# Performance work log

Hardware: AMD Instinct MI355X
Metric: run time of the kernel (lower is better)

The kernel has to match this reference:

```python
import jax, jax.numpy as jnp
import numpy as np

HEAD_DIM = 64  # scale = head_dim ** -0.5


def setup_inputs() -> dict:
    key = jax.random.key(0)
    ks = jax.random.split(key, 5)
    B, S, E = 8, 8192, 1024
    L, D = 64, 256          # n_latent_vec, latent_dim
    H = HEAD_DIM
    return {
        "input_tensor": jax.random.normal(ks[0], (B, S, E), dtype=jnp.float32),
        "latents": jax.random.normal(ks[1], (L, D), dtype=jnp.float32),
        "Wq": jax.random.normal(ks[2], (H, D), dtype=jnp.float32) * (1.0 / np.sqrt(D)),
        "Wk": jax.random.normal(ks[3], (H, E), dtype=jnp.float32) * (1.0 / np.sqrt(E)),
        "Wv": jax.random.normal(ks[4], (H, E), dtype=jnp.float32) * (1.0 / np.sqrt(E)),
    }


def reference(input_tensor, latents, Wq, Wk, Wv):
    # non-cached path, seq_len == max_seq_len so no truncation
    # queries: broadcast shared latents over batch -> [B, L, H]
    q = jnp.einsum('ld,hd->lh', latents, Wq)                 # [L, H]
    k = jnp.einsum('bse,he->bsh', input_tensor, Wk)           # [B, S, H]
    v = jnp.einsum('bse,he->bsh', input_tensor, Wv)           # [B, S, H]
    scale = HEAD_DIM ** -0.5
    scores = jnp.einsum('lh,bsh->bls', q, k) * scale          # [B, L, S]
    weights = jax.nn.softmax(scores, axis=-1)                 # dropout is identity (p=0 / eval)
    out = jnp.einsum('bls,bsh->blh', weights, v)              # [B, L, H]
    return out
```

## Files before the change

### kernel.cpp

```cpp
#include <hip/hip_runtime.h>
#include <stdint.h>


typedef __attribute__((__ext_vector_type__(4))) float f32x4;
typedef __attribute__((__ext_vector_type__(8))) short bf16x8;

__device__ __forceinline__ unsigned short f2bf(float f) {
    union { float f; uint32_t u; } v; v.f = f;
    uint32_t u = v.u;
    return (unsigned short)((u + 0x7fffu + ((u >> 16) & 1u)) >> 16);
}

__global__ __launch_bounds__(256) void prep_kernel(
    const float* __restrict__ latents, const float* __restrict__ Wq,
    const float* __restrict__ Wk, const float* __restrict__ Wv,
    unsigned short* __restrict__ wkv, unsigned short* __restrict__ qbf)
{
    const int blk = blockIdx.x, tid = threadIdx.x;
    if (blk < 128) {
        const float* src = (blk < 64) ? (Wk + (size_t)blk * 1024)
                                      : (Wv + (size_t)(blk - 64) * 1024);
        for (int i = tid; i < 1024; i += 256)
            wkv[(size_t)blk * 1024 + i] = f2bf(src[i]);
    } else {
        const int l = (blk - 128) * 4 + (tid >> 6);
        const int h = tid & 63;
        float a = 0.f;
        for (int d = 0; d < 256; ++d)
            a += latents[l * 256 + d] * Wq[h * 256 + d];
        qbf[l * 64 + h] = f2bf(a * 0.125f);
    }
}

__global__ __launch_bounds__(256) void fused_kernel(
    const float* __restrict__ x, const unsigned short* __restrict__ wkv,
    const unsigned short* __restrict__ qbf,
    float* __restrict__ Opart, float* __restrict__ mpart, float* __restrict__ spart)
{
    __shared__ unsigned short smem[33792];
    unsigned short* Ab = smem;
    unsigned short* Bb = smem + 10240;
    unsigned short* Cs = smem;
    unsigned short* qs = smem + 20480;
    unsigned short* Ps = smem + 25088;
    __shared__ float red[4][64];
    __shared__ float Mrow[64];

    const int tid = threadIdx.x;
    const int wave = tid >> 6, lane = tid & 63;
    const int g = lane >> 4, c = lane & 15;
    const int wr = wave >> 1, wc = wave & 1;
    const size_t r0 = (size_t)blockIdx.x * 128;

    {
        const int rowQ = tid >> 3, colQ = (tid & 7) * 8;
        #pragma unroll
        for (int i = 0; i < 2; ++i) {
            const int row = rowQ + 32 * i;
            *(uint4*)&qs[row * 72 + colQ] = *(const uint4*)(qbf + row * 64 + colQ);
        }
    }

    const int rowA = tid >> 3, colA = (tid & 7) * 4;
    const int rowB = tid >> 2, colB = (tid & 3) * 8;

    f32x4 acc[4][4];
    #pragma unroll
    for (int i = 0; i < 4; ++i)
        #pragma unroll
        for (int j = 0; j < 4; ++j)
            acc[i][j] = f32x4{0.f, 0.f, 0.f, 0.f};

    f32x4 areg[4];
    uint4  breg[2];

    #pragma unroll
    for (int i = 0; i < 4; ++i)
        areg[i] = *(const f32x4*)(x + (r0 + rowA + 32 * i) * 1024 + colA);
    #pragma unroll
    for (int j = 0; j < 2; ++j)
        breg[j] = *(const uint4*)(wkv + (size_t)(rowB + 64 * j) * 1024 + colB);
    #pragma unroll
    for (int i = 0; i < 4; ++i) {
        unsigned long long pk =
            (unsigned long long)f2bf(areg[i][0])        |
            ((unsigned long long)f2bf(areg[i][1]) << 16) |
            ((unsigned long long)f2bf(areg[i][2]) << 32) |
            ((unsigned long long)f2bf(areg[i][3]) << 48);
        *(unsigned long long*)&Ab[(rowA + 32 * i) * 40 + colA] = pk;
    }
    #pragma unroll
    for (int j = 0; j < 2; ++j)
        *(uint4*)&Bb[(rowB + 64 * j) * 40 + colB] = breg[j];
    __syncthreads();

    for (int t = 0; t < 32; ++t) {
        const int buf = t & 1;
        if (t < 31) {
            const int e0 = (t + 1) * 32;
            #pragma unroll
            for (int i = 0; i < 4; ++i)
                areg[i] = *(const f32x4*)(x + (r0 + rowA + 32 * i) * 1024 + e0 + colA);
            #pragma unroll
            for (int j = 0; j < 2; ++j)
                breg[j] = *(const uint4*)(wkv + (size_t)(rowB + 64 * j) * 1024 + e0 + colB);
        }
        bf16x8 af[4], bfr[4];
        #pragma unroll
        for (int ml = 0; ml < 4; ++ml)
            af[ml] = *(const bf16x8*)&Ab[(buf * 128 + 64 * wr + 16 * ml + c) * 40 + 8 * g];
        #pragma unroll
        for (int nc = 0; nc < 4; ++nc)
            bfr[nc] = *(const bf16x8*)&Bb[(buf * 128 + 64 * wc + 16 * nc + c) * 40 + 8 * g];
        #pragma unroll
        for (int ml = 0; ml < 4; ++ml)
            #pragma unroll
            for (int nc = 0; nc < 4; ++nc)
                acc[ml][nc] = __builtin_amdgcn_mfma_f32_16x16x32_bf16(
                    af[ml], bfr[nc], acc[ml][nc], 0, 0, 0);
        if (t < 31) {
            const int nb = buf ^ 1;
            #pragma unroll
            for (int i = 0; i < 4; ++i) {
                unsigned long long pk =
                    (unsigned long long)f2bf(areg[i][0])        |
                    ((unsigned long long)f2bf(areg[i][1]) << 16) |
                    ((unsigned long long)f2bf(areg[i][2]) << 32) |
                    ((unsigned long long)f2bf(areg[i][3]) << 48);
                *(unsigned long long*)&Ab[(nb * 128 + rowA + 32 * i) * 40 + colA] = pk;
            }
            #pragma unroll
            for (int j = 0; j < 2; ++j)
                *(uint4*)&Bb[(nb * 128 + rowB + 64 * j) * 40 + colB] = breg[j];
        }
        __syncthreads();
    }

    #pragma unroll
    for (int ml = 0; ml < 4; ++ml)
        #pragma unroll
        for (int nc = 0; nc < 4; ++nc)
            #pragma unroll
            for (int r = 0; r < 4; ++r)
                Cs[(64 * wr + 16 * ml + 4 * g + r) * 136 + 64 * wc + 16 * nc + c] =
                    f2bf(acc[ml][nc][r]);
    __syncthreads();

    f32x4 sc[4][2];
    #pragma unroll
    for (int ml = 0; ml < 4; ++ml)
        #pragma unroll
        for (int ns = 0; ns < 2; ++ns)
            sc[ml][ns] = f32x4{0.f, 0.f, 0.f, 0.f};
    #pragma unroll
    for (int k0 = 0; k0 < 2; ++k0) {
        bf16x8 aq[4];
        #pragma unroll
        for (int ml = 0; ml < 4; ++ml)
            aq[ml] = *(const bf16x8*)&qs[(16 * ml + c) * 72 + 32 * k0 + 8 * g];
        #pragma unroll
        for (int ns = 0; ns < 2; ++ns) {
            bf16x8 bk = *(const bf16x8*)&Cs[(32 * wave + 16 * ns + c) * 136 + 32 * k0 + 8 * g];
            #pragma unroll
            for (int ml = 0; ml < 4; ++ml)
                sc[ml][ns] = __builtin_amdgcn_mfma_f32_16x16x32_bf16(
                    aq[ml], bk, sc[ml][ns], 0, 0, 0);
        }
    }

    float mloc[4][4];
    #pragma unroll
    for (int ml = 0; ml < 4; ++ml)
        #pragma unroll
        for (int r = 0; r < 4; ++r)
            mloc[ml][r] = fmaxf(sc[ml][0][r], sc[ml][1][r]);
    #pragma unroll
    for (int off = 1; off <= 8; off <<= 1)
        #pragma unroll
        for (int ml = 0; ml < 4; ++ml)
            #pragma unroll
            for (int r = 0; r < 4; ++r)
                mloc[ml][r] = fmaxf(mloc[ml][r], __shfl_xor(mloc[ml][r], off));
    if (c == 0)
        #pragma unroll
        for (int ml = 0; ml < 4; ++ml)
            #pragma unroll
            for (int r = 0; r < 4; ++r)
                red[wave][16 * ml + 4 * g + r] = mloc[ml][r];
    __syncthreads();
    if (tid < 64) {
        float m = red[0][tid];
        m = fmaxf(m, red[1][tid]); m = fmaxf(m, red[2][tid]); m = fmaxf(m, red[3][tid]);
        Mrow[tid] = m;
    }
    __syncthreads();

    float ssum[4][4];
    #pragma unroll
    for (int ml = 0; ml < 4; ++ml)
        #pragma unroll
        for (int r = 0; r < 4; ++r)
            ssum[ml][r] = 0.f;
    #pragma unroll
    for (int ml = 0; ml < 4; ++ml)
        #pragma unroll
        for (int r = 0; r < 4; ++r) {
            const int l = 16 * ml + 4 * g + r;
            const float mr = Mrow[l];
            #pragma unroll
            for (int ns = 0; ns < 2; ++ns) {
                float p = __expf(sc[ml][ns][r] - mr);
                unsigned short pb = f2bf(p);
                Ps[l * 136 + 32 * wave + 16 * ns + c] = pb;
                union { uint32_t u; float f; } pv; pv.u = (uint32_t)pb << 16;
                ssum[ml][r] += pv.f;
            }
        }
    #pragma unroll
    for (int off = 1; off <= 8; off <<= 1)
        #pragma unroll
        for (int ml = 0; ml < 4; ++ml)
            #pragma unroll
            for (int r = 0; r < 4; ++r)
                ssum[ml][r] += __shfl_xor(ssum[ml][r], off);
    if (c == 0)
        #pragma unroll
        for (int ml = 0; ml < 4; ++ml)
            #pragma unroll
            for (int r = 0; r < 4; ++r)
                red[wave][16 * ml + 4 * g + r] = ssum[ml][r];
    __syncthreads();
    if (tid < 64) {
        const float s = red[0][tid] + red[1][tid] + red[2][tid] + red[3][tid];
        mpart[(size_t)blockIdx.x * 64 + tid] = Mrow[tid];
        spart[(size_t)blockIdx.x * 64 + tid] = s;
    }

    f32x4 o[4];
    #pragma unroll
    for (int nh = 0; nh < 4; ++nh) o[nh] = f32x4{0.f, 0.f, 0.f, 0.f};
    #pragma unroll
    for (int ks = 0; ks < 4; ++ks) {
        bf16x8 ap = *(const bf16x8*)&Ps[(16 * wave + c) * 136 + 32 * ks + 8 * g];
        #pragma unroll
        for (int nh = 0; nh < 4; ++nh) {
            bf16x8 bv;
            #pragma unroll
            for (int j = 0; j < 8; ++j)
                bv[j] = (short)Cs[(32 * ks + 8 * g + j) * 136 + 64 + 16 * nh + c];
            o[nh] = __builtin_amdgcn_mfma_f32_16x16x32_bf16(ap, bv, o[nh], 0, 0, 0);
        }
    }
    const size_t pb = (size_t)blockIdx.x * 64;
    #pragma unroll
    for (int nh = 0; nh < 4; ++nh)
        #pragma unroll
        for (int r = 0; r < 4; ++r) {
            const int l = 16 * wave + 4 * g + r;
            const int h = 16 * nh + c;
            Opart[(pb + l) * 64 + h] = o[nh][r];
        }
}

__global__ __launch_bounds__(64) void combine_kernel(
    const float* __restrict__ Opart, const float* __restrict__ mpart,
    const float* __restrict__ spart, float* __restrict__ out)
{
    const int b = blockIdx.x >> 6, l = blockIdx.x & 63, h = threadIdx.x;
    float M = -3.0e38f;
    #pragma unroll 8
    for (int ch = 0; ch < 64; ++ch)
        M = fmaxf(M, mpart[((size_t)(b * 64 + ch)) * 64 + l]);
    float den = 0.f, acc = 0.f;
    #pragma unroll 8
    for (int ch = 0; ch < 64; ++ch) {
        const size_t idx = ((size_t)(b * 64 + ch)) * 64 + l;
        const float w = __expf(mpart[idx] - M);
        den += w * spart[idx];
        acc += w * Opart[idx * 64 + h];
    }
    out[((size_t)blockIdx.x) * 64 + h] = acc / den;
}

extern "C" void kernel_launch(void* const* d_in, const int* in_sizes, int n_in,
                              void* d_out, int out_size, void* d_ws, size_t ws_size,
                              hipStream_t stream)
{
    const float* x       = (const float*)d_in[0];
    const float* latents = (const float*)d_in[1];
    const float* Wq      = (const float*)d_in[2];
    const float* Wk      = (const float*)d_in[3];
    const float* Wv      = (const float*)d_in[4];
    float* out = (float*)d_out;
    char* ws = (char*)d_ws;

    unsigned short* wkv = (unsigned short*)(ws);
    unsigned short* qbf = (unsigned short*)(ws + 262144);
    float* Opart = (float*)(ws + 270336);
    float* mpart = (float*)(ws + 270336 + 8388608);
    float* spart = (float*)(ws + 270336 + 8388608 + 131072);

    hipLaunchKernelGGL(prep_kernel, dim3(144), dim3(256), 0, stream,
                       latents, Wq, Wk, Wv, wkv, qbf);
    hipLaunchKernelGGL(fused_kernel, dim3(512), dim3(256), 0, stream,
                       x, wkv, qbf, Opart, mpart, spart);
    hipLaunchKernelGGL(combine_kernel, dim3(512), dim3(64), 0, stream,
                       Opart, mpart, spart, out);
}
```

Baseline: 81.75 us.

## Convert Wk/Wv to bf16 in-kernel, stagger K-loop start, use nontemporal x loads

The prep kernel no longer converts Wk/Wv to bf16. The fused kernel reads the fp32 weights directly and packs them to bf16 when writing them to shared memory, which removes a workspace round trip and shrinks the prep kernel to the Q projection. Each block starts its K loop at a different offset (blockIdx & 31), so concurrent blocks read different weight columns at the same time. Loads of x are marked nontemporal because that data is streamed once. The cost is twice the global bytes for the weight tiles and extra conversion ALU work in every block.

```diff
diff --git a/kernel.cpp b/kernel.cpp
--- a/kernel.cpp
+++ b/kernel.cpp
@@ -11,30 +11,33 @@
     return (unsigned short)((u + 0x7fffu + ((u >> 16) & 1u)) >> 16);
 }
 
+__device__ __forceinline__ unsigned long long pack4(f32x4 v) {
+    return (unsigned long long)f2bf(v[0])        |
+           ((unsigned long long)f2bf(v[1]) << 16) |
+           ((unsigned long long)f2bf(v[2]) << 32) |
+           ((unsigned long long)f2bf(v[3]) << 48);
+}
+
+__device__ __forceinline__ f32x4 ldnt(const float* p) {
+    return __builtin_nontemporal_load((const f32x4*)p);
+}
+
 __global__ __launch_bounds__(256) void prep_kernel(
     const float* __restrict__ latents, const float* __restrict__ Wq,
-    const float* __restrict__ Wk, const float* __restrict__ Wv,
-    unsigned short* __restrict__ wkv, unsigned short* __restrict__ qbf)
+    unsigned short* __restrict__ qbf)
 {
-    const int blk = blockIdx.x, tid = threadIdx.x;
-    if (blk < 128) {
-        const float* src = (blk < 64) ? (Wk + (size_t)blk * 1024)
-                                      : (Wv + (size_t)(blk - 64) * 1024);
-        for (int i = tid; i < 1024; i += 256)
-            wkv[(size_t)blk * 1024 + i] = f2bf(src[i]);
-    } else {
-        const int l = (blk - 128) * 4 + (tid >> 6);
-        const int h = tid & 63;
-        float a = 0.f;
-        for (int d = 0; d < 256; ++d)
-            a += latents[l * 256 + d] * Wq[h * 256 + d];
-        qbf[l * 64 + h] = f2bf(a * 0.125f);
-    }
+    const int l = blockIdx.x * 4 + (threadIdx.x >> 6);
+    const int h = threadIdx.x & 63;
+    float a = 0.f;
+    #pragma unroll 8
+    for (int d = 0; d < 256; ++d)
+        a += latents[l * 256 + d] * Wq[h * 256 + d];
+    qbf[l * 64 + h] = f2bf(a * 0.125f);
 }
 
 __global__ __launch_bounds__(256) void fused_kernel(
-    const float* __restrict__ x, const unsigned short* __restrict__ wkv,
-    const unsigned short* __restrict__ qbf,
+    const float* __restrict__ x, const float* __restrict__ Wk,
+    const float* __restrict__ Wv, const unsigned short* __restrict__ qbf,
     float* __restrict__ Opart, float* __restrict__ mpart, float* __restrict__ spart)
 {
     __shared__ unsigned short smem[33792];
@@ -51,6 +54,7 @@
     const int g = lane >> 4, c = lane & 15;
     const int wr = wave >> 1, wc = wave & 1;
     const size_t r0 = (size_t)blockIdx.x * 128;
+    const int koff = blockIdx.x & 31;
 
     {
         const int rowQ = tid >> 3, colQ = (tid & 7) * 8;
@@ -62,7 +66,7 @@
     }
 
     const int rowA = tid >> 3, colA = (tid & 7) * 4;
-    const int rowB = tid >> 2, colB = (tid & 3) * 8;
+    const int rowB = tid >> 2, qt = tid & 3;
 
     f32x4 acc[4][4];
     #pragma unroll
@@ -72,38 +76,38 @@
             acc[i][j] = f32x4{0.f, 0.f, 0.f, 0.f};
 
     f32x4 areg[4];
-    uint4  breg[2];
-
-    #pragma unroll
-    for (int i = 0; i < 4; ++i)
-        areg[i] = *(const f32x4*)(x + (r0 + rowA + 32 * i) * 1024 + colA);
-    #pragma unroll
-    for (int j = 0; j < 2; ++j)
-        breg[j] = *(const uint4*)(wkv + (size_t)(rowB + 64 * j) * 1024 + colB);
-    #pragma unroll
-    for (int i = 0; i < 4; ++i) {
-        unsigned long long pk =
-            (unsigned long long)f2bf(areg[i][0])        |
-            ((unsigned long long)f2bf(areg[i][1]) << 16) |
-            ((unsigned long long)f2bf(areg[i][2]) << 32) |
-            ((unsigned long long)f2bf(areg[i][3]) << 48);
-        *(unsigned long long*)&Ab[(rowA + 32 * i) * 40 + colA] = pk;
-    }
-    #pragma unroll
-    for (int j = 0; j < 2; ++j)
-        *(uint4*)&Bb[(rowB + 64 * j) * 40 + colB] = breg[j];
+    f32x4 bk0, bk1, bv0, bv1;
+
+    {
+        const int e0 = koff * 32;
+        #pragma unroll
+        for (int i = 0; i < 4; ++i)
+            areg[i] = ldnt(x + (r0 + rowA + 32 * i) * 1024 + e0 + colA);
+        bk0 = *(const f32x4*)(Wk + (size_t)rowB * 1024 + e0 + 8 * qt);
+        bk1 = *(const f32x4*)(Wk + (size_t)rowB * 1024 + e0 + 8 * qt + 4);
+        bv0 = *(const f32x4*)(Wv + (size_t)rowB * 1024 + e0 + 8 * qt);
+        bv1 = *(const f32x4*)(Wv + (size_t)rowB * 1024 + e0 + 8 * qt + 4);
+        #pragma unroll
+        for (int i = 0; i < 4; ++i)
+            *(unsigned long long*)&Ab[(rowA + 32 * i) * 40 + colA] = pack4(areg[i]);
+        *(unsigned long long*)&Bb[rowB * 40 + 8 * qt]       = pack4(bk0);
+        *(unsigned long long*)&Bb[rowB * 40 + 8 * qt + 4]   = pack4(bk1);
+        *(unsigned long long*)&Bb[(rowB + 64) * 40 + 8 * qt]     = pack4(bv0);
+        *(unsigned long long*)&Bb[(rowB + 64) * 40 + 8 * qt + 4] = pack4(bv1);
+    }
     __syncthreads();
 
     for (int t = 0; t < 32; ++t) {
         const int buf = t & 1;
         if (t < 31) {
-            const int e0 = (t + 1) * 32;
+            const int e0 = ((t + 1 + koff) & 31) * 32;
             #pragma unroll
             for (int i = 0; i < 4; ++i)
-                areg[i] = *(const f32x4*)(x + (r0 + rowA + 32 * i) * 1024 + e0 + colA);
-            #pragma unroll
-            for (int j = 0; j < 2; ++j)
-                breg[j] = *(const uint4*)(wkv + (size_t)(rowB + 64 * j) * 1024 + e0 + colB);
+                areg[i] = ldnt(x + (r0 + rowA + 32 * i) * 1024 + e0 + colA);
+            bk0 = *(const f32x4*)(Wk + (size_t)rowB * 1024 + e0 + 8 * qt);
+            bk1 = *(const f32x4*)(Wk + (size_t)rowB * 1024 + e0 + 8 * qt + 4);
+            bv0 = *(const f32x4*)(Wv + (size_t)rowB * 1024 + e0 + 8 * qt);
+            bv1 = *(const f32x4*)(Wv + (size_t)rowB * 1024 + e0 + 8 * qt + 4);
         }
         bf16x8 af[4], bfr[4];
         #pragma unroll
@@ -121,17 +125,13 @@
         if (t < 31) {
             const int nb = buf ^ 1;
             #pragma unroll
-            for (int i = 0; i < 4; ++i) {
-                unsigned long long pk =
-                    (unsigned long long)f2bf(areg[i][0])        |
-                    ((unsigned long long)f2bf(areg[i][1]) << 16) |
-                    ((unsigned long long)f2bf(areg[i][2]) << 32) |
-                    ((unsigned long long)f2bf(areg[i][3]) << 48);
-                *(unsigned long long*)&Ab[(nb * 128 + rowA + 32 * i) * 40 + colA] = pk;
-            }
-            #pragma unroll
-            for (int j = 0; j < 2; ++j)
-                *(uint4*)&Bb[(nb * 128 + rowB + 64 * j) * 40 + colB] = breg[j];
+            for (int i = 0; i < 4; ++i)
+                *(unsigned long long*)&Ab[(nb * 128 + rowA + 32 * i) * 40 + colA] =
+                    pack4(areg[i]);
+            *(unsigned long long*)&Bb[(nb * 128 + rowB) * 40 + 8 * qt]       = pack4(bk0);
+            *(unsigned long long*)&Bb[(nb * 128 + rowB) * 40 + 8 * qt + 4]   = pack4(bk1);
+            *(unsigned long long*)&Bb[(nb * 128 + rowB + 64) * 40 + 8 * qt]     = pack4(bv0);
+            *(unsigned long long*)&Bb[(nb * 128 + rowB + 64) * 40 + 8 * qt + 4] = pack4(bv1);
         }
         __syncthreads();
     }
@@ -294,16 +294,15 @@
     float* out = (float*)d_out;
     char* ws = (char*)d_ws;
 
-    unsigned short* wkv = (unsigned short*)(ws);
-    unsigned short* qbf = (unsigned short*)(ws + 262144);
-    float* Opart = (float*)(ws + 270336);
-    float* mpart = (float*)(ws + 270336 + 8388608);
-    float* spart = (float*)(ws + 270336 + 8388608 + 131072);
-
-    hipLaunchKernelGGL(prep_kernel, dim3(144), dim3(256), 0, stream,
-                       latents, Wq, Wk, Wv, wkv, qbf);
+    unsigned short* qbf = (unsigned short*)(ws);
+    float* Opart = (float*)(ws + 8192);
+    float* mpart = (float*)(ws + 8192 + 8388608);
+    float* spart = (float*)(ws + 8192 + 8388608 + 131072);
+
+    hipLaunchKernelGGL(prep_kernel, dim3(16), dim3(256), 0, stream,
+                       latents, Wq, qbf);
     hipLaunchKernelGGL(fused_kernel, dim3(512), dim3(256), 0, stream,
-                       x, wkv, qbf, Opart, mpart, spart);
+                       x, Wk, Wv, qbf, Opart, mpart, spart);
     hipLaunchKernelGGL(combine_kernel, dim3(512), dim3(64), 0, stream,
                        Opart, mpart, spart, out);
 }
```

Result: slower. 106.0 us (+29.7%).

## Double fused kernel threads to 512 and split the KV GEMM across eight waves

Applied to the files above, without the earlier changes.

The fused kernel now runs 512 threads (8 waves) per block instead of 256. The 128x128 projection tile is split 2x4 across waves, so each wave holds half as many accumulators and issues fewer global loads per step. This is meant to raise latency hiding and memory parallelism on the streaming fp32 input. The softmax and PV phases are guarded to run only on the first four waves, which leaves half the block idle there. The prep loop also gets an unroll pragma.

```diff
diff --git a/kernel.cpp b/kernel.cpp
--- a/kernel.cpp
+++ b/kernel.cpp
@@ -9,6 +9,13 @@
     union { float f; uint32_t u; } v; v.f = f;
     uint32_t u = v.u;
     return (unsigned short)((u + 0x7fffu + ((u >> 16) & 1u)) >> 16);
+}
+
+__device__ __forceinline__ unsigned long long pack4(f32x4 v) {
+    return (unsigned long long)f2bf(v[0])        |
+           ((unsigned long long)f2bf(v[1]) << 16) |
+           ((unsigned long long)f2bf(v[2]) << 32) |
+           ((unsigned long long)f2bf(v[3]) << 48);
 }
 
 __global__ __launch_bounds__(256) void prep_kernel(
@@ -26,13 +33,14 @@
         const int l = (blk - 128) * 4 + (tid >> 6);
         const int h = tid & 63;
         float a = 0.f;
+        #pragma unroll 8
         for (int d = 0; d < 256; ++d)
             a += latents[l * 256 + d] * Wq[h * 256 + d];
         qbf[l * 64 + h] = f2bf(a * 0.125f);
     }
 }
 
-__global__ __launch_bounds__(256) void fused_kernel(
+__global__ __launch_bounds__(512, 4) void fused_kernel(
     const float* __restrict__ x, const unsigned short* __restrict__ wkv,
     const unsigned short* __restrict__ qbf,
     float* __restrict__ Opart, float* __restrict__ mpart, float* __restrict__ spart)
@@ -49,49 +57,35 @@
     const int tid = threadIdx.x;
     const int wave = tid >> 6, lane = tid & 63;
     const int g = lane >> 4, c = lane & 15;
-    const int wr = wave >> 1, wc = wave & 1;
+    const int wr = wave >> 2, wc = wave & 3;
     const size_t r0 = (size_t)blockIdx.x * 128;
 
     {
         const int rowQ = tid >> 3, colQ = (tid & 7) * 8;
-        #pragma unroll
-        for (int i = 0; i < 2; ++i) {
-            const int row = rowQ + 32 * i;
-            *(uint4*)&qs[row * 72 + colQ] = *(const uint4*)(qbf + row * 64 + colQ);
-        }
+        *(uint4*)&qs[rowQ * 72 + colQ] = *(const uint4*)(qbf + rowQ * 64 + colQ);
     }
 
     const int rowA = tid >> 3, colA = (tid & 7) * 4;
     const int rowB = tid >> 2, colB = (tid & 3) * 8;
 
-    f32x4 acc[4][4];
+    f32x4 acc[4][2];
     #pragma unroll
     for (int i = 0; i < 4; ++i)
         #pragma unroll
-        for (int j = 0; j < 4; ++j)
+        for (int j = 0; j < 2; ++j)
             acc[i][j] = f32x4{0.f, 0.f, 0.f, 0.f};
 
-    f32x4 areg[4];
-    uint4  breg[2];
-
-    #pragma unroll
-    for (int i = 0; i < 4; ++i)
-        areg[i] = *(const f32x4*)(x + (r0 + rowA + 32 * i) * 1024 + colA);
-    #pragma unroll
-    for (int j = 0; j < 2; ++j)
-        breg[j] = *(const uint4*)(wkv + (size_t)(rowB + 64 * j) * 1024 + colB);
-    #pragma unroll
-    for (int i = 0; i < 4; ++i) {
-        unsigned long long pk =
-            (unsigned long long)f2bf(areg[i][0])        |
-            ((unsigned long long)f2bf(areg[i][1]) << 16) |
-            ((unsigned long long)f2bf(areg[i][2]) << 32) |
-            ((unsigned long long)f2bf(areg[i][3]) << 48);
-        *(unsigned long long*)&Ab[(rowA + 32 * i) * 40 + colA] = pk;
-    }
-    #pragma unroll
-    for (int j = 0; j < 2; ++j)
-        *(uint4*)&Bb[(rowB + 64 * j) * 40 + colB] = breg[j];
+    f32x4 areg[2];
+    uint4  breg;
+
+    #pragma unroll
+    for (int i = 0; i < 2; ++i)
+        areg[i] = *(const f32x4*)(x + (r0 + rowA + 64 * i) * 1024 + colA);
+    breg = *(const uint4*)(wkv + (size_t)rowB * 1024 + colB);
+    #pragma unroll
+    for (int i = 0; i < 2; ++i)
+        *(unsigned long long*)&Ab[(rowA + 64 * i) * 40 + colA] = pack4(areg[i]);
+    *(uint4*)&Bb[rowB * 40 + colB] = breg;
     __syncthreads();
 
     for (int t = 0; t < 32; ++t) {
@@ -99,39 +93,30 @@
         if (t < 31) {
             const int e0 = (t + 1) * 32;
             #pragma unroll
-            for (int i = 0; i < 4; ++i)
-                areg[i] = *(const f32x4*)(x + (r0 + rowA + 32 * i) * 1024 + e0 + colA);
-            #pragma unroll
-            for (int j = 0; j < 2; ++j)
-                breg[j] = *(const uint4*)(wkv + (size_t)(rowB + 64 * j) * 1024 + e0 + colB);
-        }
-        bf16x8 af[4], bfr[4];
+            for (int i = 0; i < 2; ++i)
+                areg[i] = *(const f32x4*)(x + (r0 + rowA + 64 * i) * 1024 + e0 + colA);
+            breg = *(const uint4*)(wkv + (size_t)rowB * 1024 + e0 + colB);
+        }
+        bf16x8 af[4], bfr[2];
         #pragma unroll
         for (int ml = 0; ml < 4; ++ml)
             af[ml] = *(const bf16x8*)&Ab[(buf * 128 + 64 * wr + 16 * ml + c) * 40 + 8 * g];
         #pragma unroll
-        for (int nc = 0; nc < 4; ++nc)
-            bfr[nc] = *(const bf16x8*)&Bb[(buf * 128 + 64 * wc + 16 * nc + c) * 40 + 8 * g];
-        #pragma unroll
-        for (int ml = 0; ml < 4; ++ml)
-            #pragma unroll
-            for (int nc = 0; nc < 4; ++nc)
+        for (int nc = 0; nc < 2; ++nc)
+            bfr[nc] = *(const bf16x8*)&Bb[(buf * 128 + 32 * wc + 16 * nc + c) * 40 + 8 * g];
+        #pragma unroll
+        for (int ml = 0; ml < 4; ++ml)
+            #pragma unroll
+            for (int nc = 0; nc < 2; ++nc)
                 acc[ml][nc] = __builtin_amdgcn_mfma_f32_16x16x32_bf16(
                     af[ml], bfr[nc], acc[ml][nc], 0, 0, 0);
         if (t < 31) {
             const int nb = buf ^ 1;
             #pragma unroll
-            for (int i = 0; i < 4; ++i) {
-                unsigned long long pk =
-                    (unsigned long long)f2bf(areg[i][0])        |
-                    ((unsigned long long)f2bf(areg[i][1]) << 16) |
-                    ((unsigned long long)f2bf(areg[i][2]) << 32) |
-                    ((unsigned long long)f2bf(areg[i][3]) << 48);
-                *(unsigned long long*)&Ab[(nb * 128 + rowA + 32 * i) * 40 + colA] = pk;
-            }
-            #pragma unroll
-            for (int j = 0; j < 2; ++j)
-                *(uint4*)&Bb[(nb * 128 + rowB + 64 * j) * 40 + colB] = breg[j];
+            for (int i = 0; i < 2; ++i)
+                *(unsigned long long*)&Ab[(nb * 128 + rowA + 64 * i) * 40 + colA] =
+                    pack4(areg[i]);
+            *(uint4*)&Bb[(nb * 128 + rowB) * 40 + colB] = breg;
         }
         __syncthreads();
     }
@@ -139,54 +124,55 @@
     #pragma unroll
     for (int ml = 0; ml < 4; ++ml)
         #pragma unroll
-        for (int nc = 0; nc < 4; ++nc)
+        for (int nc = 0; nc < 2; ++nc)
             #pragma unroll
             for (int r = 0; r < 4; ++r)
-                Cs[(64 * wr + 16 * ml + 4 * g + r) * 136 + 64 * wc + 16 * nc + c] =
+                Cs[(64 * wr + 16 * ml + 4 * g + r) * 136 + 32 * wc + 16 * nc + c] =
                     f2bf(acc[ml][nc][r]);
     __syncthreads();
 
     f32x4 sc[4][2];
-    #pragma unroll
-    for (int ml = 0; ml < 4; ++ml)
-        #pragma unroll
-        for (int ns = 0; ns < 2; ++ns)
-            sc[ml][ns] = f32x4{0.f, 0.f, 0.f, 0.f};
-    #pragma unroll
-    for (int k0 = 0; k0 < 2; ++k0) {
-        bf16x8 aq[4];
-        #pragma unroll
-        for (int ml = 0; ml < 4; ++ml)
-            aq[ml] = *(const bf16x8*)&qs[(16 * ml + c) * 72 + 32 * k0 + 8 * g];
-        #pragma unroll
-        for (int ns = 0; ns < 2; ++ns) {
-            bf16x8 bk = *(const bf16x8*)&Cs[(32 * wave + 16 * ns + c) * 136 + 32 * k0 + 8 * g];
-            #pragma unroll
-            for (int ml = 0; ml < 4; ++ml)
-                sc[ml][ns] = __builtin_amdgcn_mfma_f32_16x16x32_bf16(
-                    aq[ml], bk, sc[ml][ns], 0, 0, 0);
-        }
-    }
-
-    float mloc[4][4];
-    #pragma unroll
-    for (int ml = 0; ml < 4; ++ml)
-        #pragma unroll
-        for (int r = 0; r < 4; ++r)
-            mloc[ml][r] = fmaxf(sc[ml][0][r], sc[ml][1][r]);
-    #pragma unroll
-    for (int off = 1; off <= 8; off <<= 1)
+    if (wave < 4) {
+        #pragma unroll
+        for (int ml = 0; ml < 4; ++ml)
+            #pragma unroll
+            for (int ns = 0; ns < 2; ++ns)
+                sc[ml][ns] = f32x4{0.f, 0.f, 0.f, 0.f};
+        #pragma unroll
+        for (int k0 = 0; k0 < 2; ++k0) {
+            bf16x8 aq[4];
+            #pragma unroll
+            for (int ml = 0; ml < 4; ++ml)
+                aq[ml] = *(const bf16x8*)&qs[(16 * ml + c) * 72 + 32 * k0 + 8 * g];
+            #pragma unroll
+            for (int ns = 0; ns < 2; ++ns) {
+                bf16x8 bk = *(const bf16x8*)&Cs[(32 * wave + 16 * ns + c) * 136 + 32 * k0 + 8 * g];
+                #pragma unroll
+                for (int ml = 0; ml < 4; ++ml)
+                    sc[ml][ns] = __builtin_amdgcn_mfma_f32_16x16x32_bf16(
+                        aq[ml], bk, sc[ml][ns], 0, 0, 0);
+            }
+        }
+        float mloc[4][4];
         #pragma unroll
         for (int ml = 0; ml < 4; ++ml)
             #pragma unroll
             for (int r = 0; r < 4; ++r)
-                mloc[ml][r] = fmaxf(mloc[ml][r], __shfl_xor(mloc[ml][r], off));
-    if (c == 0)
-        #pragma unroll
-        for (int ml = 0; ml < 4; ++ml)
-            #pragma unroll
-            for (int r = 0; r < 4; ++r)
-                red[wave][16 * ml + 4 * g + r] = mloc[ml][r];
+                mloc[ml][r] = fmaxf(sc[ml][0][r], sc[ml][1][r]);
+        #pragma unroll
+        for (int off = 1; off <= 8; off <<= 1)
+            #pragma unroll
+            for (int ml = 0; ml < 4; ++ml)
+                #pragma unroll
+                for (int r = 0; r < 4; ++r)
+                    mloc[ml][r] = fmaxf(mloc[ml][r], __shfl_xor(mloc[ml][r], off));
+        if (c == 0)
+            #pragma unroll
+            for (int ml = 0; ml < 4; ++ml)
+                #pragma unroll
+                for (int r = 0; r < 4; ++r)
+                    red[wave][16 * ml + 4 * g + r] = mloc[ml][r];
+    }
     __syncthreads();
     if (tid < 64) {
         float m = red[0][tid];
@@ -195,40 +181,42 @@
     }
     __syncthreads();
 
-    float ssum[4][4];
-    #pragma unroll
-    for (int ml = 0; ml < 4; ++ml)
-        #pragma unroll
-        for (int r = 0; r < 4; ++r)
-            ssum[ml][r] = 0.f;
-    #pragma unroll
-    for (int ml = 0; ml < 4; ++ml)
-        #pragma unroll
-        for (int r = 0; r < 4; ++r) {
-            const int l = 16 * ml + 4 * g + r;
-            const float mr = Mrow[l];
-            #pragma unroll
-            for (int ns = 0; ns < 2; ++ns) {
-                float p = __expf(sc[ml][ns][r] - mr);
-                unsigned short pb = f2bf(p);
-                Ps[l * 136 + 32 * wave + 16 * ns + c] = pb;
-                union { uint32_t u; float f; } pv; pv.u = (uint32_t)pb << 16;
-                ssum[ml][r] += pv.f;
-            }
-        }
-    #pragma unroll
-    for (int off = 1; off <= 8; off <<= 1)
+    if (wave < 4) {
+        float ssum[4][4];
         #pragma unroll
         for (int ml = 0; ml < 4; ++ml)
             #pragma unroll
             for (int r = 0; r < 4; ++r)
-                ssum[ml][r] += __shfl_xor(ssum[ml][r], off);
-    if (c == 0)
-        #pragma unroll
-        for (int ml = 0; ml < 4; ++ml)
-            #pragma unroll
-            for (int r = 0; r < 4; ++r)
-                red[wave][16 * ml + 4 * g + r] = ssum[ml][r];
+                ssum[ml][r] = 0.f;
+        #pragma unroll
+        for (int ml = 0; ml < 4; ++ml)
+            #pragma unroll
+            for (int r = 0; r < 4; ++r) {
+                const int l = 16 * ml + 4 * g + r;
+                const float mr = Mrow[l];
+                #pragma unroll
+                for (int ns = 0; ns < 2; ++ns) {
+                    float p = __expf(sc[ml][ns][r] - mr);
+                    unsigned short pb = f2bf(p);
+                    Ps[l * 136 + 32 * wave + 16 * ns + c] = pb;
+                    union { uint32_t u; float f; } pv; pv.u = (uint32_t)pb << 16;
+                    ssum[ml][r] += pv.f;
+                }
+            }
+        #pragma unroll
+        for (int off = 1; off <= 8; off <<= 1)
+            #pragma unroll
+            for (int ml = 0; ml < 4; ++ml)
+                #pragma unroll
+                for (int r = 0; r < 4; ++r)
+                    ssum[ml][r] += __shfl_xor(ssum[ml][r], off);
+        if (c == 0)
+            #pragma unroll
+            for (int ml = 0; ml < 4; ++ml)
+                #pragma unroll
+                for (int r = 0; r < 4; ++r)
+                    red[wave][16 * ml + 4 * g + r] = ssum[ml][r];
+    }
     __syncthreads();
     if (tid < 64) {
         const float s = red[0][tid] + red[1][tid] + red[2][tid] + red[3][tid];
@@ -236,30 +224,32 @@
         spart[(size_t)blockIdx.x * 64 + tid] = s;
     }
 
-    f32x4 o[4];
-    #pragma unroll
-    for (int nh = 0; nh < 4; ++nh) o[nh] = f32x4{0.f, 0.f, 0.f, 0.f};
-    #pragma unroll
-    for (int ks = 0; ks < 4; ++ks) {
-        bf16x8 ap = *(const bf16x8*)&Ps[(16 * wave + c) * 136 + 32 * ks + 8 * g];
-        #pragma unroll
-        for (int nh = 0; nh < 4; ++nh) {
-            bf16x8 bv;
-            #pragma unroll
-            for (int j = 0; j < 8; ++j)
-                bv[j] = (short)Cs[(32 * ks + 8 * g + j) * 136 + 64 + 16 * nh + c];
-            o[nh] = __builtin_amdgcn_mfma_f32_16x16x32_bf16(ap, bv, o[nh], 0, 0, 0);
-        }
-    }
-    const size_t pb = (size_t)blockIdx.x * 64;
-    #pragma unroll
-    for (int nh = 0; nh < 4; ++nh)
-        #pragma unroll
-        for (int r = 0; r < 4; ++r) {
-            const int l = 16 * wave + 4 * g + r;
-            const int h = 16 * nh + c;
-            Opart[(pb + l) * 64 + h] = o[nh][r];
-        }
+    if (wave < 4) {
+        f32x4 o[4];
+        #pragma unroll
+        for (int nh = 0; nh < 4; ++nh) o[nh] = f32x4{0.f, 0.f, 0.f, 0.f};
+        #pragma unroll
+        for (int ks = 0; ks < 4; ++ks) {
+            bf16x8 ap = *(const bf16x8*)&Ps[(16 * wave + c) * 136 + 32 * ks + 8 * g];
+            #pragma unroll
+            for (int nh = 0; nh < 4; ++nh) {
+                bf16x8 bv;
+                #pragma unroll
+                for (int j = 0; j < 8; ++j)
+                    bv[j] = (short)Cs[(32 * ks + 8 * g + j) * 136 + 64 + 16 * nh + c];
+                o[nh] = __builtin_amdgcn_mfma_f32_16x16x32_bf16(ap, bv, o[nh], 0, 0, 0);
+            }
+        }
+        const size_t pb = (size_t)blockIdx.x * 64;
+        #pragma unroll
+        for (int nh = 0; nh < 4; ++nh)
+            #pragma unroll
+            for (int r = 0; r < 4; ++r) {
+                const int l = 16 * wave + 4 * g + r;
+                const int h = 16 * nh + c;
+                Opart[(pb + l) * 64 + h] = o[nh][r];
+            }
+    }
 }
 
 __global__ __launch_bounds__(64) void combine_kernel(
@@ -302,7 +292,7 @@
 
     hipLaunchKernelGGL(prep_kernel, dim3(144), dim3(256), 0, stream,
                        latents, Wq, Wk, Wv, wkv, qbf);
-    hipLaunchKernelGGL(fused_kernel, dim3(512), dim3(256), 0, stream,
+    hipLaunchKernelGGL(fused_kernel, dim3(512), dim3(512), 0, stream,
                        x, wkv, qbf, Opart, mpart, spart);
     hipLaunchKernelGGL(combine_kernel, dim3(512), dim3(64), 0, stream,
                        Opart, mpart, spart, out);
```

After: 81.85 us. Within noise of the previous version (+0.1%).

## Load MFMA operands directly from global memory, dropping LDS staging

Applied to the files above, without the earlier changes.

The K/V projection GEMM loop no longer stages x and the bf16 weights through double-buffered shared memory. Each wave now loads its MFMA fragments straight from global memory into registers, converts fp32 to bf16 in registers, and processes two K-steps per iteration with no __syncthreads. This removes LDS traffic and barriers but duplicates global loads across the waves that share rows or columns, which leans on L1/L2 hits, and raises register use. Launch bounds now request 2 blocks per SM and the prep dot-product loop is unrolled.

```diff
diff --git a/kernel.cpp b/kernel.cpp
--- a/kernel.cpp
+++ b/kernel.cpp
@@ -9,6 +9,13 @@
     union { float f; uint32_t u; } v; v.f = f;
     uint32_t u = v.u;
     return (unsigned short)((u + 0x7fffu + ((u >> 16) & 1u)) >> 16);
+}
+
+__device__ __forceinline__ unsigned long long pack4(f32x4 v) {
+    return (unsigned long long)f2bf(v[0])        |
+           ((unsigned long long)f2bf(v[1]) << 16) |
+           ((unsigned long long)f2bf(v[2]) << 32) |
+           ((unsigned long long)f2bf(v[3]) << 48);
 }
 
 __global__ __launch_bounds__(256) void prep_kernel(
@@ -26,20 +33,19 @@
         const int l = (blk - 128) * 4 + (tid >> 6);
         const int h = tid & 63;
         float a = 0.f;
+        #pragma unroll 8
         for (int d = 0; d < 256; ++d)
             a += latents[l * 256 + d] * Wq[h * 256 + d];
         qbf[l * 64 + h] = f2bf(a * 0.125f);
     }
 }
 
-__global__ __launch_bounds__(256) void fused_kernel(
+__global__ __launch_bounds__(256, 2) void fused_kernel(
     const float* __restrict__ x, const unsigned short* __restrict__ wkv,
     const unsigned short* __restrict__ qbf,
     float* __restrict__ Opart, float* __restrict__ mpart, float* __restrict__ spart)
 {
     __shared__ unsigned short smem[33792];
-    unsigned short* Ab = smem;
-    unsigned short* Bb = smem + 10240;
     unsigned short* Cs = smem;
     unsigned short* qs = smem + 20480;
     unsigned short* Ps = smem + 25088;
@@ -61,8 +67,14 @@
         }
     }
 
-    const int rowA = tid >> 3, colA = (tid & 7) * 4;
-    const int rowB = tid >> 2, colB = (tid & 3) * 8;
+    const float* xA[4];
+    const unsigned short* wB[4];
+    #pragma unroll
+    for (int ml = 0; ml < 4; ++ml)
+        xA[ml] = x + (r0 + 64 * wr + 16 * ml + c) * 1024 + 8 * g;
+    #pragma unroll
+    for (int nc = 0; nc < 4; ++nc)
+        wB[nc] = wkv + (size_t)(64 * wc + 16 * nc + c) * 1024 + 8 * g;
 
     f32x4 acc[4][4];
     #pragma unroll
@@ -71,69 +83,58 @@
         for (int j = 0; j < 4; ++j)
             acc[i][j] = f32x4{0.f, 0.f, 0.f, 0.f};
 
-    f32x4 areg[4];
-    uint4  breg[2];
-
-    #pragma unroll
-    for (int i = 0; i < 4; ++i)
-        areg[i] = *(const f32x4*)(x + (r0 + rowA + 32 * i) * 1024 + colA);
-    #pragma unroll
-    for (int j = 0; j < 2; ++j)
-        breg[j] = *(const uint4*)(wkv + (size_t)(rowB + 64 * j) * 1024 + colB);
-    #pragma unroll
-    for (int i = 0; i < 4; ++i) {
-        unsigned long long pk =
-            (unsigned long long)f2bf(areg[i][0])        |
-            ((unsigned long long)f2bf(areg[i][1]) << 16) |
-            ((unsigned long long)f2bf(areg[i][2]) << 32) |
-            ((unsigned long long)f2bf(areg[i][3]) << 48);
-        *(unsigned long long*)&Ab[(rowA + 32 * i) * 40 + colA] = pk;
-    }
-    #pragma unroll
-    for (int j = 0; j < 2; ++j)
-        *(uint4*)&Bb[(rowB + 64 * j) * 40 + colB] = breg[j];
-    __syncthreads();
-
-    for (int t = 0; t < 32; ++t) {
-        const int buf = t & 1;
-        if (t < 31) {
-            const int e0 = (t + 1) * 32;
-            #pragma unroll
-            for (int i = 0; i < 4; ++i)
-                areg[i] = *(const f32x4*)(x + (r0 + rowA + 32 * i) * 1024 + e0 + colA);
-            #pragma unroll
-            for (int j = 0; j < 2; ++j)
-                breg[j] = *(const uint4*)(wkv + (size_t)(rowB + 64 * j) * 1024 + e0 + colB);
-        }
-        bf16x8 af[4], bfr[4];
-        #pragma unroll
-        for (int ml = 0; ml < 4; ++ml)
-            af[ml] = *(const bf16x8*)&Ab[(buf * 128 + 64 * wr + 16 * ml + c) * 40 + 8 * g];
+    f32x4 lo0[4], hi0[4], lo1[4], hi1[4];
+    uint4  br0[4], br1[4];
+
+    for (int t = 0; t < 32; t += 2) {
+        const int e0 = t * 32;
+        #pragma unroll
+        for (int ml = 0; ml < 4; ++ml) {
+            lo0[ml] = *(const f32x4*)(xA[ml] + e0);
+            hi0[ml] = *(const f32x4*)(xA[ml] + e0 + 4);
+        }
         #pragma unroll
         for (int nc = 0; nc < 4; ++nc)
-            bfr[nc] = *(const bf16x8*)&Bb[(buf * 128 + 64 * wc + 16 * nc + c) * 40 + 8 * g];
-        #pragma unroll
-        for (int ml = 0; ml < 4; ++ml)
-            #pragma unroll
-            for (int nc = 0; nc < 4; ++nc)
-                acc[ml][nc] = __builtin_amdgcn_mfma_f32_16x16x32_bf16(
-                    af[ml], bfr[nc], acc[ml][nc], 0, 0, 0);
-        if (t < 31) {
-            const int nb = buf ^ 1;
-            #pragma unroll
-            for (int i = 0; i < 4; ++i) {
-                unsigned long long pk =
-                    (unsigned long long)f2bf(areg[i][0])        |
-                    ((unsigned long long)f2bf(areg[i][1]) << 16) |
-                    ((unsigned long long)f2bf(areg[i][2]) << 32) |
-                    ((unsigned long long)f2bf(areg[i][3]) << 48);
-                *(unsigned long long*)&Ab[(nb * 128 + rowA + 32 * i) * 40 + colA] = pk;
+            br0[nc] = *(const uint4*)(wB[nc] + e0);
+        #pragma unroll
+        for (int ml = 0; ml < 4; ++ml) {
+            lo1[ml] = *(const f32x4*)(xA[ml] + e0 + 32);
+            hi1[ml] = *(const f32x4*)(xA[ml] + e0 + 36);
+        }
+        #pragma unroll
+        for (int nc = 0; nc < 4; ++nc)
+            br1[nc] = *(const uint4*)(wB[nc] + e0 + 32);
+
+        {
+            bf16x8 af[4];
+            #pragma unroll
+            for (int ml = 0; ml < 4; ++ml) {
+                union { unsigned long long u[2]; bf16x8 v; } w;
+                w.u[0] = pack4(lo0[ml]); w.u[1] = pack4(hi0[ml]);
+                af[ml] = w.v;
             }
             #pragma unroll
-            for (int j = 0; j < 2; ++j)
-                *(uint4*)&Bb[(nb * 128 + rowB + 64 * j) * 40 + colB] = breg[j];
-        }
-        __syncthreads();
+            for (int ml = 0; ml < 4; ++ml)
+                #pragma unroll
+                for (int nc = 0; nc < 4; ++nc)
+                    acc[ml][nc] = __builtin_amdgcn_mfma_f32_16x16x32_bf16(
+                        af[ml], *(const bf16x8*)&br0[nc], acc[ml][nc], 0, 0, 0);
+        }
+        {
+            bf16x8 af[4];
+            #pragma unroll
+            for (int ml = 0; ml < 4; ++ml) {
+                union { unsigned long long u[2]; bf16x8 v; } w;
+                w.u[0] = pack4(lo1[ml]); w.u[1] = pack4(hi1[ml]);
+                af[ml] = w.v;
+            }
+            #pragma unroll
+            for (int ml = 0; ml < 4; ++ml)
+                #pragma unroll
+                for (int nc = 0; nc < 4; ++nc)
+                    acc[ml][nc] = __builtin_amdgcn_mfma_f32_16x16x32_bf16(
+                        af[ml], *(const bf16x8*)&br1[nc], acc[ml][nc], 0, 0, 0);
+        }
     }
 
     #pragma unroll
```

Measured after the change: 125.1 us. +53.0%, slower.
